# Optimization experiments

Measured on AMD Instinct MI355X. Metric: run time of the kernel, lower is better.

## Reference

```python
import jax, jax.numpy as jnp
import numpy as np

DIM = 1024
HEADS = 8
DIM_HEAD = 64
EPS = 1e-10
LN_EPS = 1e-5


def setup_inputs() -> dict:
    key = jax.random.key(0)
    k1, k2, k3 = jax.random.split(key, 3)
    b, n = 2, 4096
    x = jax.random.normal(k1, (b, n, DIM), dtype=jnp.float32)
    ln_gamma = jnp.ones((DIM,), dtype=jnp.float32)
    ln_beta = jnp.zeros((DIM,), dtype=jnp.float32)
    w_qkv = jax.random.normal(k2, (DIM, 3 * HEADS * DIM_HEAD), dtype=jnp.float32) * (DIM ** -0.5)
    w_out = jax.random.normal(k3, (HEADS * DIM_HEAD, DIM), dtype=jnp.float32) * ((HEADS * DIM_HEAD) ** -0.5)
    return {"x": x, "ln_gamma": ln_gamma, "ln_beta": ln_beta, "w_qkv": w_qkv, "w_out": w_out}


def _layernorm(x, gamma, beta):
    mu = jnp.mean(x, axis=-1, keepdims=True)
    var = jnp.var(x, axis=-1, keepdims=True)
    return (x - mu) * jax.lax.rsqrt(var + LN_EPS) * gamma + beta


def reference(x, ln_gamma, ln_beta, w_qkv, w_out):
    b, n, _ = x.shape
    h, dh = HEADS, DIM_HEAD
    scale = dh ** -0.5

    xn = _layernorm(x, ln_gamma, ln_beta)          # prenorm
    qkv = xn @ w_qkv                               # [b, n, 3*h*dh]
    q, k, v = jnp.split(qkv, 3, axis=-1)
    # [b, n, h*dh] -> [b, h, n, dh]
    def to_heads(t):
        return t.reshape(b, n, h, dh).transpose(0, 2, 1, 3)
    q, k, v = to_heads(q), to_heads(k), to_heads(v)

    # Ring/blockwise attention with online softmax is mathematically
    # equivalent to full softmax attention with an eps in the denominator.
    sim = jnp.einsum('bhid,bhjd->bhij', q, k) * scale   # [b, h, n, n]
    causal_mask = jnp.tril(jnp.ones((n, n), dtype=bool))
    sim = jnp.where(causal_mask, sim, -jnp.finfo(sim.dtype).max)

    m = jnp.max(sim, axis=-1, keepdims=True)            # row max (stable)
    p = jnp.exp(sim - m)
    denom = jnp.sum(p, axis=-1, keepdims=True) + EPS
    attn = p / denom

    out = jnp.einsum('bhij,bhjd->bhid', attn, v)        # [b, h, n, dh]
    out = out.transpose(0, 2, 1, 3).reshape(b, n, h * dh)
    return out @ w_out                                  # [b, n, dim]
```

## Files before the change

### kernel.cpp

```cpp
#include <hip/hip_runtime.h>
#include <hip/hip_bf16.h>
#include <stdint.h>

typedef unsigned short u16;
typedef unsigned int u32;

typedef __attribute__((ext_vector_type(8))) __bf16 bf16x8;
typedef __attribute__((ext_vector_type(4))) float f32x4;
typedef __attribute__((ext_vector_type(8))) u16 u16x8;

#define DIM 1024
#define SEQ 4096
#define NTOK 8192
#define NBH 16
#define NSLOT 136

static __device__ __forceinline__ float bf2f(u16 u) {
    union { u32 u; float f; } c; c.u = ((u32)u) << 16; return c.f;
}
static __device__ __forceinline__ u16 f2bf(float f) {
    union { float f; u32 u; } c; c.f = f;
    u32 u = c.u;
    return (u16)((u + 0x7FFF + ((u >> 16) & 1)) >> 16);
}
static __device__ __forceinline__ u16 cvt_bf16(float f) {
    union { __bf16 b; u16 u; } c; c.b = (__bf16)f;
    return c.u;
}
static __device__ __forceinline__ u32 pack_bf16(float lo, float hi) {
    return (u32)cvt_bf16(lo) | ((u32)cvt_bf16(hi) << 16);
}
static __device__ __forceinline__ f32x4 mfma_bf16(bf16x8 a, bf16x8 b, f32x4 c) {
    return __builtin_amdgcn_mfma_f32_16x16x32_bf16(a, b, c, 0, 0, 0);
}

typedef const __attribute__((address_space(1))) unsigned int* gptr_t;
typedef __attribute__((address_space(3))) unsigned int* lptr_t;

__global__ __launch_bounds__(256) void prep_kernel(const float* __restrict__ x,
                                                   const float* __restrict__ g,
                                                   const float* __restrict__ bta,
                                                   u16* __restrict__ xn,
                                                   const float* __restrict__ wqkv,
                                                   u16* __restrict__ wqkvT,
                                                   const float* __restrict__ wout,
                                                   u16* __restrict__ woutT) {
    __shared__ float red[8];
    __shared__ float tT[32][33];
    int bid = blockIdx.x;
    int tid = threadIdx.x;

    if (bid < NTOK) {
        int row = bid;
        float4 v = ((const float4*)(x + (size_t)row * DIM))[tid];
        float f[4] = {v.x, v.y, v.z, v.w};
        float s = 0.f, s2 = 0.f;
#pragma unroll
        for (int i = 0; i < 4; i++) { s += f[i]; s2 += f[i] * f[i]; }
#pragma unroll
        for (int m = 1; m < 64; m <<= 1) { s += __shfl_xor(s, m); s2 += __shfl_xor(s2, m); }
        int w = tid >> 6;
        if ((tid & 63) == 0) { red[w * 2] = s; red[w * 2 + 1] = s2; }
        __syncthreads();
        s  = red[0] + red[2] + red[4] + red[6];
        s2 = red[1] + red[3] + red[5] + red[7];
        float mu = s * (1.f / DIM);
        float var = s2 * (1.f / DIM) - mu * mu;
        float rstd = rsqrtf(var + 1e-5f);
        u16 o[4];
#pragma unroll
        for (int i = 0; i < 4; i++) {
            int c = tid * 4 + i;
            o[i] = f2bf((f[i] - mu) * rstd * g[c] + bta[c]);
        }
        *(uint64_t*)(xn + (size_t)row * DIM + tid * 4) = *(uint64_t*)o;
        return;
    }

    int tt = bid - NTOK;
    const float* src; u16* dst; int R, C, bx, by;
    if (tt < 1536) { src = wqkv; dst = wqkvT; R = 1024; C = 1536; bx = tt % 48; by = tt / 48; }
    else { tt -= 1536; src = wout; dst = woutT; R = 512; C = 1024; bx = tt & 31; by = tt >> 5; }
    int lx = tid & 31, ly = tid >> 5;
    int c = bx * 32 + lx;
#pragma unroll
    for (int i = 0; i < 32; i += 8)
        tT[ly + i][lx] = src[(size_t)(by * 32 + ly + i) * C + c];
    __syncthreads();
    int rr = by * 32 + lx;
#pragma unroll
    for (int i = 0; i < 32; i += 8)
        dst[(size_t)(bx * 32 + ly + i) * R + rr] = f2bf(tT[lx][ly + i]);
}

template <int K>
static __device__ __forceinline__ void gemm_core(const u16* __restrict__ A,
                                                 const u16* __restrict__ B,
                                                 int rowBase, int colBase,
                                                 u16* A_lds, u16* B_lds,
                                                 f32x4 acc[4][4]) {
    int tid = threadIdx.x;
    int lane = tid & 63;
    int l15 = lane & 15, q4 = lane >> 4;
    int w = tid >> 6;
    int wm = w >> 1, wn = w & 1;
#pragma unroll
    for (int mt = 0; mt < 4; mt++)
#pragma unroll
        for (int nt = 0; nt < 4; nt++) acc[mt][nt] = (f32x4){0.f, 0.f, 0.f, 0.f};

    char* Ab = (char*)A_lds;
    char* Bb = (char*)B_lds;

    for (int k0 = 0; k0 < K; k0 += 32) {
        __syncthreads();
#pragma unroll
        for (int i = 0; i < 2; i++) {
            int c = i * 256 + tid;
            int r = c >> 2;
            int piece = (c & 3) * 8;
            const u16* gA = A + (size_t)(rowBase + r) * K + k0 + piece;
            const u16* gB = B + (size_t)(colBase + r) * K + k0 + piece;
            unsigned ldsOff = (unsigned)(i * 4096 + w * 1024);
            __builtin_amdgcn_global_load_lds((gptr_t)gA, (lptr_t)(Ab + ldsOff), 16, 0, 0);
            __builtin_amdgcn_global_load_lds((gptr_t)gB, (lptr_t)(Bb + ldsOff), 16, 0, 0);
        }
        __syncthreads();
        bf16x8 a[4], b[4];
#pragma unroll
        for (int mt = 0; mt < 4; mt++)
            a[mt] = *(const bf16x8*)(A_lds + (wm * 64 + mt * 16 + l15) * 32 + q4 * 8);
#pragma unroll
        for (int nt = 0; nt < 4; nt++)
            b[nt] = *(const bf16x8*)(B_lds + (wn * 64 + nt * 16 + l15) * 32 + q4 * 8);
#pragma unroll
        for (int mt = 0; mt < 4; mt++)
#pragma unroll
            for (int nt = 0; nt < 4; nt++)
                acc[mt][nt] = mfma_bf16(a[mt], b[nt], acc[mt][nt]);
    }
}

__global__ __launch_bounds__(256) void gemm_qkv_kernel(const u16* __restrict__ xn,
                                                       const u16* __restrict__ wT,
                                                       u16* __restrict__ qb,
                                                       u16* __restrict__ kb,
                                                       u16* __restrict__ vbT) {
    __shared__ u16 A_lds[128 * 32];
    __shared__ u16 B_lds[128 * 32];
    f32x4 acc[4][4];
    gemm_core<1024>(xn, wT, blockIdx.x * 128, blockIdx.y * 128, A_lds, B_lds, acc);
    int lane = threadIdx.x & 63;
    int w = threadIdx.x >> 6;
    int wm = w >> 1, wn = w & 1;
    const float SC = 0.125f * 1.44269504f;
#pragma unroll
    for (int mt = 0; mt < 4; mt++) {
#pragma unroll
        for (int nt = 0; nt < 4; nt++) {
#pragma unroll
            for (int r = 0; r < 4; r++) {
                int m = blockIdx.x * 128 + wm * 64 + mt * 16 + (lane >> 4) * 4 + r;
                int n = blockIdx.y * 128 + wn * 64 + nt * 16 + (lane & 15);
                int piece = n >> 9;
                int c = n & 511;
                int h = c >> 6;
                int d = c & 63;
                int bi = m >> 12;
                int nn = m & 4095;
                int bh = bi * 8 + h;
                float av = acc[mt][nt][r];
                if (piece == 0)      qb[((size_t)(bh * SEQ + nn) << 6) + d] = f2bf(av * SC);
                else if (piece == 1) kb[((size_t)(bh * SEQ + nn) << 6) + d] = f2bf(av);
                else                 vbT[((size_t)(bh * 64 + d) << 12) + nn] = f2bf(av);
            }
        }
    }
}

__global__ __launch_bounds__(256) void gemm_out_kernel(const u16* __restrict__ aout,
                                                       const u16* __restrict__ wT,
                                                       float* __restrict__ out) {
    __shared__ u16 A_lds[128 * 32];
    __shared__ u16 B_lds[128 * 32];
    f32x4 acc[4][4];
    gemm_core<512>(aout, wT, blockIdx.x * 128, blockIdx.y * 128, A_lds, B_lds, acc);
    int lane = threadIdx.x & 63;
    int w = threadIdx.x >> 6;
    int wm = w >> 1, wn = w & 1;
#pragma unroll
    for (int mt = 0; mt < 4; mt++) {
#pragma unroll
        for (int nt = 0; nt < 4; nt++) {
#pragma unroll
            for (int r = 0; r < 4; r++) {
                int m = blockIdx.x * 128 + wm * 64 + mt * 16 + (lane >> 4) * 4 + r;
                int n = blockIdx.y * 128 + wn * 64 + nt * 16 + (lane & 15);
                out[(size_t)m * DIM + n] = acc[mt][nt][r];
            }
        }
    }
}


__global__ __launch_bounds__(128) void attn_partial_kernel(const u16* __restrict__ qb,
                                                           const u16* __restrict__ kb,
                                                           const u16* __restrict__ vbT,
                                                           u16* __restrict__ part,
                                                           float* __restrict__ lpart) {
    __shared__ u16 K_lds[4096];
    __shared__ u16 V_lds[4096];
    __shared__ u16 P_lds[2][1024];

    int bid = blockIdx.x;
    int bs = (bid & 7) * 272 + (bid >> 3);
    int idx = NBH * NSLOT - 1 - bs;
    int bh = idx / NSLOT;
    int s  = idx - bh * NSLOT;
    int qt, ci;
    if (s < 20)       { qt = s; ci = 0; }
    else if (s < 60)  { int t = s - 20;  qt = 20 + (t >> 1); ci = t & 1; }
    else if (s < 120) { int t = s - 60;  qt = 40 + t / 3;    ci = t - (t / 3) * 3; }
    else              { int t = s - 120; qt = 60 + (t >> 2); ci = t & 3; }
    int nq = qt + 1;
    int nc = (nq + 19) / 20;
    int L  = nq / nc;
    int R  = nq - L * nc;
    int kt0 = ci * L + (ci < R ? ci : R);
    int kt1 = kt0 + L + (ci < R ? 1 : 0) - 1;

    int tid = threadIdx.x;
    int lane = tid & 63;
    int l15 = lane & 15, g = lane >> 4;
    int w = tid >> 6;
    int swz = (l15 & 7) << 3;
    int rd0 = (g * 8) ^ swz;
    int rd1 = (32 + g * 8) ^ swz;

    const u16* Kp0 = kb + (size_t)bh * SEQ * 64;
    const u16* VTp = vbT + (size_t)bh * 64 * SEQ;

    bf16x8 bQ[2][2];
#pragma unroll
    for (int qs = 0; qs < 2; qs++) {
        const u16* qp = qb + ((size_t)bh * SEQ + (size_t)qt * 64 + w * 32 + qs * 16 + l15) * 64;
        bQ[qs][0] = *(const bf16x8*)(qp + g * 8);
        bQ[qs][1] = *(const bf16x8*)(qp + 32 + g * 8);
    }

    int wcc[4], soK[4];
    size_t soV[4];
#pragma unroll
    for (int i = 0; i < 4; i++) {
        int c = tid + 128 * i;
        int r = c >> 3, gg = c & 7;
        wcc[i] = r * 64 + ((gg ^ (r & 7)) * 8);
        soK[i] = r * 64 + gg * 8;
        soV[i] = (size_t)r * SEQ + gg * 8;
    }

    u16x8 krA[4], vrA[4];
    {
        const u16* Kt = Kp0 + (size_t)kt0 * 4096;
#pragma unroll
        for (int i = 0; i < 4; i++) {
            krA[i] = *(const u16x8*)(Kt + soK[i]);
            vrA[i] = *(const u16x8*)(VTp + soV[i] + kt0 * 64);
        }
    }

    f32x4 Oacc[2][4];
    f32x4 l_acc[2];
#pragma unroll
    for (int qs = 0; qs < 2; qs++) {
        l_acc[qs] = (f32x4){0.f, 0.f, 0.f, 0.f};
#pragma unroll
        for (int vt = 0; vt < 4; vt++) Oacc[qs][vt] = (f32x4){0.f, 0.f, 0.f, 0.f};
    }

    const __bf16 one_bf = (__bf16)1.0f;
    bf16x8 vones = {one_bf, one_bf, one_bf, one_bf, one_bf, one_bf, one_bf, one_bf};

    u16* Pw = &P_lds[w][0];

    for (int kt = kt0; kt <= kt1; kt++) {
        __syncthreads();
#pragma unroll
        for (int i = 0; i < 4; i++) {
            *(u16x8*)(K_lds + wcc[i]) = krA[i];
            *(u16x8*)(V_lds + wcc[i]) = vrA[i];
        }
        __syncthreads();
        int ktn = (kt < kt1) ? kt + 1 : kt1;
        {
            const u16* Ktn = Kp0 + (size_t)ktn * 4096;
#pragma unroll
            for (int i = 0; i < 4; i++) {
                krA[i] = *(const u16x8*)(Ktn + soK[i]);
                vrA[i] = *(const u16x8*)(VTp + soV[i] + ktn * 64);
            }
        }

        bf16x8 ka[4][2];
#pragma unroll
        for (int nt = 0; nt < 4; nt++) {
            int row = nt * 16 + l15;
            ka[nt][0] = *(const bf16x8*)(K_lds + row * 64 + rd0);
            ka[nt][1] = *(const bf16x8*)(K_lds + row * 64 + rd1);
        }

        bf16x8 aP[2][2];
#pragma unroll
        for (int qs = 0; qs < 2; qs++) {
            f32x4 sv[4];
#pragma unroll
            for (int nt = 0; nt < 4; nt++) {
                f32x4 z = (f32x4){0.f, 0.f, 0.f, 0.f};
                z = mfma_bf16(ka[nt][0], bQ[qs][0], z);
                z = mfma_bf16(ka[nt][1], bQ[qs][1], z);
                sv[nt] = z;
            }

            if (kt != qt) {
#pragma unroll
                for (int nt = 0; nt < 4; nt++) {
                    uint2 t;
                    t.x = pack_bf16(__builtin_amdgcn_exp2f(sv[nt][0]),
                                    __builtin_amdgcn_exp2f(sv[nt][1]));
                    t.y = pack_bf16(__builtin_amdgcn_exp2f(sv[nt][2]),
                                    __builtin_amdgcn_exp2f(sv[nt][3]));
                    *(uint2*)(Pw + l15 * 64 + ((nt * 16 + g * 4) ^ swz)) = t;
                }
            } else {
                int qg = w * 32 + qs * 16 + l15;
#pragma unroll
                for (int nt = 0; nt < 4; nt++) {
                    float p[4];
#pragma unroll
                    for (int r = 0; r < 4; r++) {
                        int kg = nt * 16 + g * 4 + r;
                        p[r] = (kg <= qg) ? __builtin_amdgcn_exp2f(sv[nt][r]) : 0.f;
                    }
                    uint2 t;
                    t.x = pack_bf16(p[0], p[1]);
                    t.y = pack_bf16(p[2], p[3]);
                    *(uint2*)(Pw + l15 * 64 + ((nt * 16 + g * 4) ^ swz)) = t;
                }
            }

            aP[qs][0] = *(const bf16x8*)(Pw + l15 * 64 + rd0);
            aP[qs][1] = *(const bf16x8*)(Pw + l15 * 64 + rd1);
            l_acc[qs] = mfma_bf16(aP[qs][0], vones, l_acc[qs]);
            l_acc[qs] = mfma_bf16(aP[qs][1], vones, l_acc[qs]);
        }

#pragma unroll
        for (int vt = 0; vt < 4; vt++) {
            int vrow = vt * 16 + l15;
            bf16x8 bV0 = *(const bf16x8*)(V_lds + vrow * 64 + rd0);
            bf16x8 bV1 = *(const bf16x8*)(V_lds + vrow * 64 + rd1);
#pragma unroll
            for (int qs = 0; qs < 2; qs++) {
                Oacc[qs][vt] = mfma_bf16(aP[qs][0], bV0, Oacc[qs][vt]);
                Oacc[qs][vt] = mfma_bf16(aP[qs][1], bV1, Oacc[qs][vt]);
            }
        }
    }

    u16* po = part + (size_t)idx * 4096;
#pragma unroll
    for (int qs = 0; qs < 2; qs++) {
#pragma unroll
        for (int vt = 0; vt < 4; vt++)
#pragma unroll
            for (int r = 0; r < 4; r++) {
                int q = w * 32 + qs * 16 + g * 4 + r;
                int d = vt * 16 + l15;
                po[q * 64 + d] = f2bf(Oacc[qs][vt][r]);
            }
        if (l15 == 0) {
#pragma unroll
            for (int r = 0; r < 4; r++)
                lpart[(size_t)idx * 64 + w * 32 + qs * 16 + g * 4 + r] = l_acc[qs][r];
        }
    }
}

__global__ __launch_bounds__(256) void attn_combine_kernel(const u16* __restrict__ part,
                                                           const float* __restrict__ lpart,
                                                           u16* __restrict__ aout) {
    int bid = blockIdx.x;
    int bh = bid >> 6;
    int qt = bid & 63;
    int nc, base;
    if (qt < 20)      { nc = 1; base = qt; }
    else if (qt < 40) { nc = 2; base = 20 + (qt - 20) * 2; }
    else if (qt < 60) { nc = 3; base = 60 + (qt - 40) * 3; }
    else              { nc = 4; base = 120 + (qt - 60) * 4; }
    int sb = bh * NSLOT + base;

    int t = threadIdx.x;
    int q = t >> 2;
    int dg = (t & 3) * 16;

    float acc[16];
#pragma unroll
    for (int j = 0; j < 16; j++) acc[j] = 0.f;
    float ll = 0.f;
    for (int ci = 0; ci < nc; ci++) {
        const u16* pp = part + (size_t)(sb + ci) * 4096 + q * 64 + dg;
        u16x8 v0 = *(const u16x8*)pp;
        u16x8 v1 = *(const u16x8*)(pp + 8);
#pragma unroll
        for (int j = 0; j < 8; j++) { acc[j] += bf2f(v0[j]); acc[8 + j] += bf2f(v1[j]); }
        ll += lpart[(size_t)(sb + ci) * 64 + q];
    }
    float inv = 1.f / (ll + 1e-10f);
    int b = bh >> 3, h = bh & 7;
    size_t row = (size_t)(b * SEQ + qt * 64 + q);
    u16 o[16];
#pragma unroll
    for (int j = 0; j < 16; j++) o[j] = f2bf(acc[j] * inv);
    u16* dst = aout + row * 512 + h * 64 + dg;
    *(u16x8*)dst = *(u16x8*)o;
    *(u16x8*)(dst + 8) = *(u16x8*)(o + 8);
}

extern "C" void kernel_launch(void* const* d_in, const int* in_sizes, int n_in,
                              void* d_out, int out_size, void* d_ws, size_t ws_size,
                              hipStream_t stream) {
    const float* x    = (const float*)d_in[0];
    const float* g    = (const float*)d_in[1];
    const float* bta  = (const float*)d_in[2];
    const float* wqkv = (const float*)d_in[3];
    const float* wout = (const float*)d_in[4];
    float* out = (float*)d_out;

    char* ws = (char*)d_ws;
    size_t off = 0;
    auto alloc = [&](size_t bytes) {
        void* p = ws + off;
        off += (bytes + 255) & ~(size_t)255;
        return p;
    };
    u16* xn    = (u16*)alloc((size_t)NTOK * DIM * 2);
    u16* wqkvT = (u16*)alloc((size_t)1536 * 1024 * 2);
    u16* woutT = (u16*)alloc((size_t)1024 * 512 * 2);
    u16* qb    = (u16*)alloc((size_t)NBH * SEQ * 64 * 2);
    u16* kb    = (u16*)alloc((size_t)NBH * SEQ * 64 * 2);
    u16* vbT   = (u16*)alloc((size_t)NBH * SEQ * 64 * 2);
    u16* part  = xn;
    float* lpart = (float*)(xn + (size_t)NBH * NSLOT * 4096);
    u16* aout  = qb;

    prep_kernel<<<NTOK + 1536 + 512, 256, 0, stream>>>(x, g, bta, xn, wqkv, wqkvT, wout, woutT);
    gemm_qkv_kernel<<<dim3(64, 12), 256, 0, stream>>>(xn, wqkvT, qb, kb, vbT);
    attn_partial_kernel<<<NBH * NSLOT, 128, 0, stream>>>(qb, kb, vbT, part, lpart);
    attn_combine_kernel<<<NBH * 64, 256, 0, stream>>>(part, lpart, aout);
    gemm_out_kernel<<<dim3(64, 8), 256, 0, stream>>>(aout, woutT, out);
}
```

Before: 210.4 us.

## Load K/V tiles directly to LDS and process two key tiles per sync

Replaces the register-staged K/V prefetch with global_load_lds direct-to-LDS transfers. Each iteration now loads two 64-key tiles into double LDS buffers, then computes both, halving the barrier count per key tile. The cost is that loads are no longer overlapped with compute: the second barrier waits for both tiles to arrive before any math starts. LDS usage also doubles.

Result: no change. 214.0 us (+1.7%).

```diff
diff --git a/kernel.cpp b/kernel.cpp
--- a/kernel.cpp
+++ b/kernel.cpp
@@ -208,9 +208,9 @@
                                                            const u16* __restrict__ vbT,
                                                            u16* __restrict__ part,
                                                            float* __restrict__ lpart) {
-    __shared__ u16 K_lds[4096];
-    __shared__ u16 V_lds[4096];
-    __shared__ u16 P_lds[2][1024];
+    __shared__ u16 K_lds[2][4096];
+    __shared__ u16 V_lds[2][4096];
+    __shared__ u16 P_lds[2][2][1024];
 
     int bid = blockIdx.x;
     int bs = (bid & 7) * 272 + (bid >> 3);
@@ -248,26 +248,8 @@
         bQ[qs][1] = *(const bf16x8*)(qp + 32 + g * 8);
     }
 
-    int wcc[4], soK[4];
-    size_t soV[4];
-#pragma unroll
-    for (int i = 0; i < 4; i++) {
-        int c = tid + 128 * i;
-        int r = c >> 3, gg = c & 7;
-        wcc[i] = r * 64 + ((gg ^ (r & 7)) * 8);
-        soK[i] = r * 64 + gg * 8;
-        soV[i] = (size_t)r * SEQ + gg * 8;
-    }
-
-    u16x8 krA[4], vrA[4];
-    {
-        const u16* Kt = Kp0 + (size_t)kt0 * 4096;
-#pragma unroll
-        for (int i = 0; i < 4; i++) {
-            krA[i] = *(const u16x8*)(Kt + soK[i]);
-            vrA[i] = *(const u16x8*)(VTp + soV[i] + kt0 * 64);
-        }
-    }
+    int rloc = lane >> 3;
+    int sgr  = ((lane & 7) ^ ((lane >> 3) & 7)) * 8;
 
     f32x4 Oacc[2][4];
     f32x4 l_acc[2];
@@ -281,88 +263,103 @@
     const __bf16 one_bf = (__bf16)1.0f;
     bf16x8 vones = {one_bf, one_bf, one_bf, one_bf, one_bf, one_bf, one_bf, one_bf};
 
-    u16* Pw = &P_lds[w][0];
-
-    for (int kt = kt0; kt <= kt1; kt++) {
+    for (int kt = kt0; kt <= kt1; kt += 2) {
         __syncthreads();
-#pragma unroll
-        for (int i = 0; i < 4; i++) {
-            *(u16x8*)(K_lds + wcc[i]) = krA[i];
-            *(u16x8*)(V_lds + wcc[i]) = vrA[i];
+        {
+            const u16* Kt = Kp0 + (size_t)kt * 4096;
+#pragma unroll
+            for (int o = 0; o < 4; o++) {
+                int rb = w * 32 + o * 8;
+                __builtin_amdgcn_global_load_lds((gptr_t)(Kt + (rb + rloc) * 64 + sgr),
+                                                 (lptr_t)((char*)&K_lds[0][0] + rb * 128), 16, 0, 0);
+                __builtin_amdgcn_global_load_lds((gptr_t)(VTp + (size_t)(rb + rloc) * SEQ + kt * 64 + sgr),
+                                                 (lptr_t)((char*)&V_lds[0][0] + rb * 128), 16, 0, 0);
+            }
+        }
+        if (kt + 1 <= kt1) {
+            const u16* Kt = Kp0 + (size_t)(kt + 1) * 4096;
+#pragma unroll
+            for (int o = 0; o < 4; o++) {
+                int rb = w * 32 + o * 8;
+                __builtin_amdgcn_global_load_lds((gptr_t)(Kt + (rb + rloc) * 64 + sgr),
+                                                 (lptr_t)((char*)&K_lds[1][0] + rb * 128), 16, 0, 0);
+                __builtin_amdgcn_global_load_lds((gptr_t)(VTp + (size_t)(rb + rloc) * SEQ + (kt + 1) * 64 + sgr),
+                                                 (lptr_t)((char*)&V_lds[1][0] + rb * 128), 16, 0, 0);
+            }
         }
         __syncthreads();
-        int ktn = (kt < kt1) ? kt + 1 : kt1;
-        {
-            const u16* Ktn = Kp0 + (size_t)ktn * 4096;
-#pragma unroll
-            for (int i = 0; i < 4; i++) {
-                krA[i] = *(const u16x8*)(Ktn + soK[i]);
-                vrA[i] = *(const u16x8*)(VTp + soV[i] + ktn * 64);
-            }
-        }
-
-        bf16x8 ka[4][2];
-#pragma unroll
-        for (int nt = 0; nt < 4; nt++) {
-            int row = nt * 16 + l15;
-            ka[nt][0] = *(const bf16x8*)(K_lds + row * 64 + rd0);
-            ka[nt][1] = *(const bf16x8*)(K_lds + row * 64 + rd1);
-        }
-
-        bf16x8 aP[2][2];
-#pragma unroll
-        for (int qs = 0; qs < 2; qs++) {
-            f32x4 sv[4];
+
+#pragma unroll
+        for (int tp = 0; tp < 2; tp++) {
+            int ktx = kt + tp;
+            if (ktx > kt1) break;
+            const u16* KL = &K_lds[tp][0];
+            const u16* VL = &V_lds[tp][0];
+            u16* Pw = &P_lds[w][tp][0];
+
+            bf16x8 ka[4][2];
 #pragma unroll
             for (int nt = 0; nt < 4; nt++) {
-                f32x4 z = (f32x4){0.f, 0.f, 0.f, 0.f};
-                z = mfma_bf16(ka[nt][0], bQ[qs][0], z);
-                z = mfma_bf16(ka[nt][1], bQ[qs][1], z);
-                sv[nt] = z;
-            }
-
-            if (kt != qt) {
+                int row = nt * 16 + l15;
+                ka[nt][0] = *(const bf16x8*)(KL + row * 64 + rd0);
+                ka[nt][1] = *(const bf16x8*)(KL + row * 64 + rd1);
+            }
+
+            bf16x8 aP[2][2];
+#pragma unroll
+            for (int qs = 0; qs < 2; qs++) {
+                f32x4 sv[4];
 #pragma unroll
                 for (int nt = 0; nt < 4; nt++) {
-                    uint2 t;
-                    t.x = pack_bf16(__builtin_amdgcn_exp2f(sv[nt][0]),
-                                    __builtin_amdgcn_exp2f(sv[nt][1]));
-                    t.y = pack_bf16(__builtin_amdgcn_exp2f(sv[nt][2]),
-                                    __builtin_amdgcn_exp2f(sv[nt][3]));
-                    *(uint2*)(Pw + l15 * 64 + ((nt * 16 + g * 4) ^ swz)) = t;
+                    f32x4 z = (f32x4){0.f, 0.f, 0.f, 0.f};
+                    z = mfma_bf16(ka[nt][0], bQ[qs][0], z);
+                    z = mfma_bf16(ka[nt][1], bQ[qs][1], z);
+                    sv[nt] = z;
                 }
-            } else {
-                int qg = w * 32 + qs * 16 + l15;
-#pragma unroll
-                for (int nt = 0; nt < 4; nt++) {
-                    float p[4];
-#pragma unroll
-                    for (int r = 0; r < 4; r++) {
-                        int kg = nt * 16 + g * 4 + r;
-                        p[r] = (kg <= qg) ? __builtin_amdgcn_exp2f(sv[nt][r]) : 0.f;
+
+                if (ktx != qt) {
+#pragma unroll
+                    for (int nt = 0; nt < 4; nt++) {
+                        uint2 t;
+                        t.x = pack_bf16(__builtin_amdgcn_exp2f(sv[nt][0]),
+                                        __builtin_amdgcn_exp2f(sv[nt][1]));
+                        t.y = pack_bf16(__builtin_amdgcn_exp2f(sv[nt][2]),
+                                        __builtin_amdgcn_exp2f(sv[nt][3]));
+                        *(uint2*)(Pw + l15 * 64 + ((nt * 16 + g * 4) ^ swz)) = t;
                     }
-                    uint2 t;
-                    t.x = pack_bf16(p[0], p[1]);
-                    t.y = pack_bf16(p[2], p[3]);
-                    *(uint2*)(Pw + l15 * 64 + ((nt * 16 + g * 4) ^ swz)) = t;
+                } else {
+                    int qg = w * 32 + qs * 16 + l15;
+#pragma unroll
+                    for (int nt = 0; nt < 4; nt++) {
+                        float p[4];
+#pragma unroll
+                        for (int r = 0; r < 4; r++) {
+                            int kg = nt * 16 + g * 4 + r;
+                            p[r] = (kg <= qg) ? __builtin_amdgcn_exp2f(sv[nt][r]) : 0.f;
+                        }
+                        uint2 t;
+                        t.x = pack_bf16(p[0], p[1]);
+                        t.y = pack_bf16(p[2], p[3]);
+                        *(uint2*)(Pw + l15 * 64 + ((nt * 16 + g * 4) ^ swz)) = t;
+                    }
                 }
-            }
-
-            aP[qs][0] = *(const bf16x8*)(Pw + l15 * 64 + rd0);
-            aP[qs][1] = *(const bf16x8*)(Pw + l15 * 64 + rd1);
-            l_acc[qs] = mfma_bf16(aP[qs][0], vones, l_acc[qs]);
-            l_acc[qs] = mfma_bf16(aP[qs][1], vones, l_acc[qs]);
-        }
-
-#pragma unroll
-        for (int vt = 0; vt < 4; vt++) {
-            int vrow = vt * 16 + l15;
-            bf16x8 bV0 = *(const bf16x8*)(V_lds + vrow * 64 + rd0);
-            bf16x8 bV1 = *(const bf16x8*)(V_lds + vrow * 64 + rd1);
-#pragma unroll
-            for (int qs = 0; qs < 2; qs++) {
-                Oacc[qs][vt] = mfma_bf16(aP[qs][0], bV0, Oacc[qs][vt]);
-                Oacc[qs][vt] = mfma_bf16(aP[qs][1], bV1, Oacc[qs][vt]);
+
+                aP[qs][0] = *(const bf16x8*)(Pw + l15 * 64 + rd0);
+                aP[qs][1] = *(const bf16x8*)(Pw + l15 * 64 + rd1);
+                l_acc[qs] = mfma_bf16(aP[qs][0], vones, l_acc[qs]);
+                l_acc[qs] = mfma_bf16(aP[qs][1], vones, l_acc[qs]);
+            }
+
+#pragma unroll
+            for (int vt = 0; vt < 4; vt++) {
+                int vrow = vt * 16 + l15;
+                bf16x8 bV0 = *(const bf16x8*)(VL + vrow * 64 + rd0);
+                bf16x8 bV1 = *(const bf16x8*)(VL + vrow * 64 + rd1);
+#pragma unroll
+                for (int qs = 0; qs < 2; qs++) {
+                    Oacc[qs][vt] = mfma_bf16(aP[qs][0], bV0, Oacc[qs][vt]);
+                    Oacc[qs][vt] = mfma_bf16(aP[qs][1], bV1, Oacc[qs][vt]);
+                }
             }
         }
     }
```
